# Kernel optimization log

Measured on AMD Instinct MI355X. Metric: run time of the kernel, lower is better.

The kernel has to match this reference:

```python
import jax, jax.numpy as jnp
import numpy as np
import math

T, N, D, H = 1024, 8, 1024, 16
HD = D // H  # head_dim = 64


def setup_inputs() -> dict:
    key = jax.random.key(0)
    k1, k2, k3, k4 = jax.random.split(key, 4)
    scale = 1.0 / math.sqrt(D)  # roughly xavier-scale params
    return {
        "x": jax.random.normal(k1, (T, N, D), dtype=jnp.float32),
        "q_weight": jax.random.normal(k2, (D, H, HD), dtype=jnp.float32) * scale,
        "v_weight": jax.random.normal(k3, (D, H, HD), dtype=jnp.float32) * scale,
        "out_w": jax.random.normal(k4, (D, D), dtype=jnp.float32) * scale,
        "out_b": jnp.zeros((D,), dtype=jnp.float32),
    }


def reference(x, q_weight, v_weight, out_w, out_b):
    inv_sqrt_hd = 1.0 / math.sqrt(HD)
    # q = k : (T, N, H, HD)
    q = jnp.einsum('tbm,mhd->tbhd', x, q_weight)
    q_sq = jnp.einsum('tbhd,tbhd->tbh', q, q)  # squared norms
    # squared L2 distance logits: (T, S, N, H)
    squared_dist = q_sq[:, None] + q_sq[None, :] - 2.0 * jnp.einsum('tbhd,sbhd->tsbh', q, q)
    attn_logits = -squared_dist * inv_sqrt_hd
    attn_weights = jax.nn.softmax(attn_logits, axis=1)  # softmax over source dim S
    # A = W_q W_q^T per head: (H, D, D)
    A = jnp.einsum('mhd,nhd->hmn', q_weight, q_weight) * inv_sqrt_hd
    XA = jnp.einsum('tbm,hmn->tbhn', x, A)           # (T, N, H, D)
    PXA = jnp.einsum('tsbh,sbhm->tbhm', attn_weights, XA)  # (T, N, H, D)
    PXAV = jnp.einsum('tbhm,mhd->tbhd', PXA, v_weight).reshape(T, N, D)
    return PXAV @ out_w.T + out_b
```

## Files before the change

### kernel.cpp

```cpp
#include <hip/hip_runtime.h>
#include <hip/hip_bf16.h>

#define T_ 1024
#define N_ 8
#define D_ 1024
#define H_ 16
#define HD_ 64

typedef __attribute__((ext_vector_type(8))) short bf16x8;
typedef __attribute__((ext_vector_type(4))) float f32x4;
typedef __attribute__((ext_vector_type(16))) float f32x16;
typedef __attribute__((ext_vector_type(4))) int i32x4;
typedef __attribute__((ext_vector_type(2))) int i32x2;
typedef unsigned short u16;
typedef unsigned int u32;

__device__ __forceinline__ float bf2f(u16 u){
  union { float f; unsigned int i; } v; v.i = ((unsigned int)u) << 16; return v.f;
}
__device__ __forceinline__ u16 f2bf(float f){
  union { float f; unsigned int i; } v; v.f = f;
  unsigned int r = v.i + 0x7FFFu + ((v.i >> 16) & 1u);
  return (u16)(r >> 16);
}
__device__ __forceinline__ u16 f2bf_fast(float f){
  __hip_bfloat16 h = __float2bfloat16(f);
  return *reinterpret_cast<u16*>(&h);
}
__device__ __forceinline__ float exp2_raw(float x){
  float r;
  asm("v_exp_f32 %0, %1" : "=v"(r) : "v"(x));
  return r;
}
__device__ __forceinline__ void gl_lds16(const u16* g, u16* l){
  __builtin_amdgcn_global_load_lds(
      (const __attribute__((address_space(1))) unsigned int*)g,
      (__attribute__((address_space(3))) unsigned int*)(unsigned int)(unsigned long long)l,
      16, 0, 0);
}

__global__ __launch_bounds__(256) void k_wqt(const float* __restrict__ Wq, u16* __restrict__ Wqt){
  __shared__ float tld[64][65];
  int m0 = blockIdx.x * 64, n0 = blockIdx.y * 64;
  int col = threadIdx.x & 63, rq = threadIdx.x >> 6;
  #pragma unroll
  for (int p = 0; p < 16; ++p){
    int row = rq * 16 + p;
    tld[row][col] = Wq[(size_t)(m0 + row) * D_ + n0 + col];
  }
  __syncthreads();
  #pragma unroll
  for (int p = 0; p < 16; ++p){
    int row = rq * 16 + p;
    Wqt[(size_t)(n0 + row) * D_ + m0 + col] = f2bf(tld[col][row]);
  }
}

__global__ __launch_bounds__(256) void k_bmatp(const float* __restrict__ qw, const float* __restrict__ vw,
                                               float* __restrict__ Bp){
  int h = (int)blockIdx.x >> 3, sp = (int)blockIdx.x & 7;
  int tid = threadIdx.x, lane = tid & 63, w = tid >> 6;
  int g = lane >> 4, c = lane & 15;
  __shared__ u16 Qt[64 * 72];
  __shared__ u16 Vt[64 * 72];
  f32x4 zero = {0.f, 0.f, 0.f, 0.f};
  f32x4 acc[4];
  #pragma unroll
  for (int eb = 0; eb < 4; ++eb) acc[eb] = zero;
  int m = tid >> 2, cg = tid & 3;
  for (int mt = sp * 128; mt < sp * 128 + 128; mt += 64){
    __syncthreads();
    #pragma unroll
    for (int q = 0; q < 4; ++q){
      int e0 = cg * 16 + q * 4;
      f32x4 vq = *(const f32x4*)(qw + (size_t)(mt + m) * D_ + h * 64 + e0);
      f32x4 vv = *(const f32x4*)(vw + (size_t)(mt + m) * D_ + h * 64 + e0);
      #pragma unroll
      for (int j = 0; j < 4; ++j){
        Qt[(e0 + j) * 72 + m] = f2bf_fast(vq[j]);
        Vt[(e0 + j) * 72 + m] = f2bf_fast(vv[j]);
      }
    }
    __syncthreads();
    #pragma unroll
    for (int kk = 0; kk < 2; ++kk){
      bf16x8 av = *(const bf16x8*)&Vt[(w * 16 + c) * 72 + kk * 32 + g * 8];
      #pragma unroll
      for (int eb = 0; eb < 4; ++eb){
        bf16x8 bq = *(const bf16x8*)&Qt[(eb * 16 + c) * 72 + kk * 32 + g * 8];
        acc[eb] = __builtin_amdgcn_mfma_f32_16x16x32_bf16(av, bq, acc[eb], 0, 0, 0);
      }
    }
  }
  #pragma unroll
  for (int eb = 0; eb < 4; ++eb)
    #pragma unroll
    for (int r = 0; r < 4; ++r){
      int d = w * 16 + g * 4 + r, e = eb * 16 + c;
      Bp[(((size_t)sp * 16 + h) * 64 + d) * 64 + e] = acc[eb][r];
    }
}

__global__ __launch_bounds__(256) void k_bred(const float* __restrict__ Bp, u16* __restrict__ Bt){
  int i = blockIdx.x * 256 + threadIdx.x;
  float s = 0.f;
  #pragma unroll
  for (int j = 0; j < 8; ++j) s += Bp[(size_t)j * 65536 + i];
  Bt[i] = f2bf(s * 0.125f);
}

__device__ __forceinline__ int swz(int row, int colbyte){
  return row * 64 + (((colbyte) ^ ((row & 7) << 4)) >> 1);
}

template<int A_F32, int B_F32, int EPI>
__global__ __launch_bounds__(256) void k_gemm(const void* __restrict__ A_, const void* __restrict__ B_,
                                              void* __restrict__ Cv, const float* __restrict__ bias,
                                              int M, int N, int K){
  int nbn = N >> 7;
  int ii = (int)blockIdx.x;
  int sw = (ii & 7) * 64 + (ii >> 3);
  int bm = sw / nbn, bn = sw % nbn;
  int tid = threadIdx.x, lane = tid & 63, wid = tid >> 6;
  int wr = wid >> 1, wc = wid & 1, g = lane >> 4, c = lane & 15;
  __shared__ u16 As[2][128 * 64];
  __shared__ u16 Bs[2][128 * 64];
  int srow[4], scol[4], sdst[4];
  #pragma unroll
  for (int p = 0; p < 4; ++p){
    int slot = (wid * 4 + p) * 64 + lane;
    int row = slot >> 3, c8 = slot & 7;
    srow[p] = row;
    scol[p] = (c8 ^ (row & 7)) * 8;
    sdst[p] = slot * 8;
  }
  int rrow[4], rc8[4];
  #pragma unroll
  for (int p = 0; p < 4; ++p){
    int ci = tid + p * 256;
    rrow[p] = ci >> 3; rc8[p] = ci & 7;
  }
  f32x4 zero = {0.f, 0.f, 0.f, 0.f};
  f32x4 acc[4][4];
  #pragma unroll
  for (int m = 0; m < 4; ++m)
    #pragma unroll
    for (int n = 0; n < 4; ++n) acc[m][n] = zero;
  f32x4 rA[4][2], rB[4][2];
  const u16* Ab = (const u16*)A_;
  const u16* Bb = (const u16*)B_;
  const float* Af = (const float*)A_;
  const float* Bf = (const float*)B_;
  if (!A_F32){
    #pragma unroll
    for (int p = 0; p < 4; ++p)
      gl_lds16(Ab + (size_t)(bm * 128 + srow[p]) * K + scol[p], &As[0][sdst[p]]);
  }
  if (!B_F32){
    #pragma unroll
    for (int p = 0; p < 4; ++p)
      gl_lds16(Bb + (size_t)(bn * 128 + srow[p]) * K + scol[p], &Bs[0][sdst[p]]);
  }
  if (A_F32){
    #pragma unroll
    for (int p = 0; p < 4; ++p){
      const float* src = Af + (size_t)(bm * 128 + rrow[p]) * K + rc8[p] * 8;
      rA[p][0] = *(const f32x4*)src;
      rA[p][1] = *(const f32x4*)(src + 4);
    }
    #pragma unroll
    for (int p = 0; p < 4; ++p){
      union { u16 u[8]; i32x4 v; } pk;
      #pragma unroll
      for (int j = 0; j < 4; ++j){ pk.u[j] = f2bf_fast(rA[p][0][j]); pk.u[4 + j] = f2bf_fast(rA[p][1][j]); }
      *(i32x4*)&As[0][swz(rrow[p], rc8[p] * 16)] = pk.v;
    }
  }
  if (B_F32){
    #pragma unroll
    for (int p = 0; p < 4; ++p){
      const float* src = Bf + (size_t)(bn * 128 + rrow[p]) * K + rc8[p] * 8;
      rB[p][0] = *(const f32x4*)src;
      rB[p][1] = *(const f32x4*)(src + 4);
    }
    #pragma unroll
    for (int p = 0; p < 4; ++p){
      union { u16 u[8]; i32x4 v; } pk;
      #pragma unroll
      for (int j = 0; j < 4; ++j){ pk.u[j] = f2bf_fast(rB[p][0][j]); pk.u[4 + j] = f2bf_fast(rB[p][1][j]); }
      *(i32x4*)&Bs[0][swz(rrow[p], rc8[p] * 16)] = pk.v;
    }
  }
  int NT = K >> 6;
  int cur = 0;
  for (int st = 0; st < NT; ++st){
    __syncthreads();
    int kt1 = (st + 1) * 64;
    int nb = cur ^ 1;
    if (st + 1 < NT){
      if (!A_F32){
        #pragma unroll
        for (int p = 0; p < 4; ++p)
          gl_lds16(Ab + (size_t)(bm * 128 + srow[p]) * K + kt1 + scol[p], &As[nb][sdst[p]]);
      }
      if (!B_F32){
        #pragma unroll
        for (int p = 0; p < 4; ++p)
          gl_lds16(Bb + (size_t)(bn * 128 + srow[p]) * K + kt1 + scol[p], &Bs[nb][sdst[p]]);
      }
      if (A_F32){
        #pragma unroll
        for (int p = 0; p < 4; ++p){
          const float* src = Af + (size_t)(bm * 128 + rrow[p]) * K + kt1 + rc8[p] * 8;
          rA[p][0] = *(const f32x4*)src;
          rA[p][1] = *(const f32x4*)(src + 4);
        }
      }
      if (B_F32){
        #pragma unroll
        for (int p = 0; p < 4; ++p){
          const float* src = Bf + (size_t)(bn * 128 + rrow[p]) * K + kt1 + rc8[p] * 8;
          rB[p][0] = *(const f32x4*)src;
          rB[p][1] = *(const f32x4*)(src + 4);
        }
      }
    }
    #pragma unroll
    for (int kk = 0; kk < 2; ++kk){
      bf16x8 af[4], bfr[4];
      #pragma unroll
      for (int m = 0; m < 4; ++m){
        int row = wr * 64 + m * 16 + c;
        af[m] = *(const bf16x8*)&As[cur][swz(row, kk * 64 + g * 16)];
      }
      #pragma unroll
      for (int n = 0; n < 4; ++n){
        int row = wc * 64 + n * 16 + c;
        bfr[n] = *(const bf16x8*)&Bs[cur][swz(row, kk * 64 + g * 16)];
      }
      #pragma unroll
      for (int m = 0; m < 4; ++m)
        #pragma unroll
        for (int n = 0; n < 4; ++n)
          acc[m][n] = __builtin_amdgcn_mfma_f32_16x16x32_bf16(af[m], bfr[n], acc[m][n], 0, 0, 0);
    }
    if (st + 1 < NT){
      if (A_F32){
        #pragma unroll
        for (int p = 0; p < 4; ++p){
          union { u16 u[8]; i32x4 v; } pk;
          #pragma unroll
          for (int j = 0; j < 4; ++j){ pk.u[j] = f2bf_fast(rA[p][0][j]); pk.u[4 + j] = f2bf_fast(rA[p][1][j]); }
          *(i32x4*)&As[nb][swz(rrow[p], rc8[p] * 16)] = pk.v;
        }
      }
      if (B_F32){
        #pragma unroll
        for (int p = 0; p < 4; ++p){
          union { u16 u[8]; i32x4 v; } pk;
          #pragma unroll
          for (int j = 0; j < 4; ++j){ pk.u[j] = f2bf_fast(rB[p][0][j]); pk.u[4 + j] = f2bf_fast(rB[p][1][j]); }
          *(i32x4*)&Bs[nb][swz(rrow[p], rc8[p] * 16)] = pk.v;
        }
      }
    }
    cur ^= 1;
  }
  #pragma unroll
  for (int m = 0; m < 4; ++m)
    #pragma unroll
    for (int n = 0; n < 4; ++n)
      #pragma unroll
      for (int r = 0; r < 4; ++r){
        int row = bm * 128 + wr * 64 + m * 16 + g * 4 + r;
        int col = bn * 128 + wc * 64 + n * 16 + c;
        float v = acc[m][n][r];
        if (EPI == 0){
          int t = row >> 3, b = row & 7, hh = col >> 6, dd = col & 63;
          ((u16*)Cv)[(((size_t)(b * H_ + hh)) * T_ + t) * HD_ + dd] = f2bf(v);
        } else {
          ((float*)Cv)[(size_t)row * N + col] = v + bias[col];
        }
      }
}

__global__ __launch_bounds__(256) void k_u(const u16* __restrict__ qb, const u16* __restrict__ Bt,
                                           u16* __restrict__ ubt, float* __restrict__ qsq){
  int blk = (int)blockIdx.x;
  int bh = blk >> 2;
  int w = threadIdx.x >> 6;
  int tt = (blk & 3) * 4 + w;
  int h = bh & 15, t0 = tt * 64;
  int lane = threadIdx.x & 63, g = lane >> 4, c = lane & 15;
  const float QS_SCALE = 0.125f * 1.44269504088896340736f;
  bf16x8 af[4][2], bq[4][2];
  #pragma unroll
  for (int mf = 0; mf < 4; ++mf)
    #pragma unroll
    for (int kk = 0; kk < 2; ++kk)
      af[mf][kk] = *(const bf16x8*)(Bt + ((size_t)(h * 64 + mf * 16 + c)) * 64 + kk * 32 + g * 8);
  #pragma unroll
  for (int nf = 0; nf < 4; ++nf)
    #pragma unroll
    for (int kk = 0; kk < 2; ++kk)
      bq[nf][kk] = *(const bf16x8*)(qb + ((size_t)(bh * 1024 + t0 + nf * 16 + c)) * 64 + kk * 32 + g * 8);
  #pragma unroll
  for (int nf = 0; nf < 4; ++nf){
    float ss = 0.f;
    #pragma unroll
    for (int kk = 0; kk < 2; ++kk)
      #pragma unroll
      for (int j = 0; j < 8; ++j){ float f = bf2f((u16)bq[nf][kk][j]); ss = fmaf(f, f, ss); }
    ss += __shfl_xor(ss, 16);
    ss += __shfl_xor(ss, 32);
    if (lane < 16) qsq[(size_t)bh * 1024 + t0 + nf * 16 + lane] = ss * QS_SCALE;
  }
  f32x4 zero = {0.f, 0.f, 0.f, 0.f};
  f32x4 acc[4][4];
  #pragma unroll
  for (int mf = 0; mf < 4; ++mf)
    #pragma unroll
    for (int nf = 0; nf < 4; ++nf) acc[mf][nf] = zero;
  #pragma unroll
  for (int kk = 0; kk < 2; ++kk)
    #pragma unroll
    for (int mf = 0; mf < 4; ++mf)
      #pragma unroll
      for (int nf = 0; nf < 4; ++nf)
        acc[mf][nf] = __builtin_amdgcn_mfma_f32_16x16x32_bf16(af[mf][kk], bq[nf][kk], acc[mf][nf], 0, 0, 0);
  #pragma unroll
  for (int mf = 0; mf < 4; ++mf)
    #pragma unroll
    for (int nf = 0; nf < 4; ++nf)
      #pragma unroll
      for (int r = 0; r < 4; ++r)
        ubt[((size_t)(bh * 64 + mf * 16 + g * 4 + r)) * 1024 + t0 + nf * 16 + c] = f2bf(acc[mf][nf][r]);
}

__global__ __launch_bounds__(256, 4) void k_attn(const u16* __restrict__ qb, const u16* __restrict__ ubt,
                                                 const float* __restrict__ qsq, u16* __restrict__ obm){
  int i = (int)blockIdx.x;
  int bh = ((i & 7) << 4) + (i >> 6);
  int tt = (i >> 3) & 7;
  int b = bh >> 4, h = bh & 15;
  int tid = threadIdx.x, w = tid >> 6, lane = tid & 63;
  int lo = lane & 31, hi = lane >> 5;
  __shared__ u16 Kl[2][64 * 64];
  __shared__ u16 Ul[2][64 * 64];
  __shared__ float Qs[1024];
  const float C1 = 0.25f * 1.44269504088896340736f;
  int t0 = tt * 128 + w * 32;
  const u16* qbh = qb + (size_t)bh * 65536;
  const u16* ubh = ubt + (size_t)bh * 65536;
  const float* qsb = qsq + (size_t)bh * 1024;
  *(f32x4*)&Qs[tid * 4] = *(const f32x4*)(qsb + tid * 4);
  bf16x8 qB[4];
  #pragma unroll
  for (int kd = 0; kd < 4; ++kd)
    qB[kd] = *(const bf16x8*)(qbh + (t0 + lo) * 64 + kd * 16 + hi * 8);
  f32x16 o0 = {0,0,0,0,0,0,0,0,0,0,0,0,0,0,0,0};
  f32x16 o1 = {0,0,0,0,0,0,0,0,0,0,0,0,0,0,0,0};
  const f32x16 zero16 = {0,0,0,0,0,0,0,0,0,0,0,0,0,0,0,0};
  float l_c = 0.f;
  int slot0 = (w * 2 + 0) * 64 + lane, slot1 = (w * 2 + 1) * 64 + lane;
  int r0 = slot0 >> 3, sc0 = ((slot0 & 7) ^ (r0 & 7)) * 8;
  int r1 = slot1 >> 3, sc1 = ((slot1 & 7) ^ (r1 & 7)) * 8;
  int d0 = (w * 2 + 0) * 512, d1 = (w * 2 + 1) * 512;
  gl_lds16(qbh + r0 * 64 + sc0, &Kl[0][d0]);
  gl_lds16(qbh + r1 * 64 + sc1, &Kl[0][d1]);
  gl_lds16(ubh + (size_t)r0 * 1024 + sc0, &Ul[0][d0]);
  gl_lds16(ubh + (size_t)r1 * 1024 + sc1, &Ul[0][d1]);
  int cur = 0;
  for (int st = 0; st < 16; ++st){
    int s0 = st * 64;
    __syncthreads();
    if (st < 15){
      int s1 = s0 + 64;
      int nb = cur ^ 1;
      gl_lds16(qbh + (s1 + r0) * 64 + sc0, &Kl[nb][d0]);
      gl_lds16(qbh + (s1 + r1) * 64 + sc1, &Kl[nb][d1]);
      gl_lds16(ubh + (size_t)r0 * 1024 + s1 + sc0, &Ul[nb][d0]);
      gl_lds16(ubh + (size_t)r1 * 1024 + s1 + sc1, &Ul[nb][d1]);
    }
    const u16* Kc = &Kl[cur][0];
    const u16* Uc = &Ul[cur][0];
    #pragma unroll
    for (int ts = 0; ts < 2; ++ts){
      f32x16 sf = zero16;
      __builtin_amdgcn_s_setprio(1);
      #pragma unroll
      for (int kd = 0; kd < 4; ++kd){
        bf16x8 kA = *(const bf16x8*)&Kc[swz(ts * 32 + lo, kd * 32 + hi * 16)];
        sf = __builtin_amdgcn_mfma_f32_32x32x16_bf16(kA, qB[kd], sf, 0, 0, 0);
      }
      __builtin_amdgcn_s_setprio(0);
      f32x4 qs_[4];
      #pragma unroll
      for (int q = 0; q < 4; ++q)
        qs_[q] = *(const f32x4*)&Qs[s0 + ts * 32 + q * 8 + hi * 4];
      float p[16];
      #pragma unroll
      for (int r = 0; r < 16; ++r)
        p[r] = exp2_raw(fmaf(sf[r], C1, -qs_[r >> 2][r & 3]));
      float sA = ((p[0] + p[1]) + (p[2] + p[3])) + ((p[4] + p[5]) + (p[6] + p[7]));
      float sB = ((p[8] + p[9]) + (p[10] + p[11])) + ((p[12] + p[13]) + (p[14] + p[15]));
      l_c += sA + sB;
      u32 W[8];
      #pragma unroll
      for (int q = 0; q < 8; ++q)
        W[q] = ((u32)f2bf_fast(p[2 * q + 1]) << 16) | (u32)f2bf_fast(p[2 * q]);
      #pragma unroll
      for (int ml = 0; ml < 2; ++ml){
        int m_g = ts * 2 + ml;
        int base = ml * 4;
        i32x2 sw0 = __builtin_amdgcn_permlane32_swap((int)W[base + 0], (int)W[base + 2], false, false);
        i32x2 sw1 = __builtin_amdgcn_permlane32_swap((int)W[base + 1], (int)W[base + 3], false, false);
        union { u32 wd[4]; bf16x8 v; } pa;
        pa.wd[0] = (u32)sw0[0]; pa.wd[1] = (u32)sw1[0]; pa.wd[2] = (u32)sw0[1]; pa.wd[3] = (u32)sw1[1];
        bf16x8 u0 = *(const bf16x8*)&Uc[swz(lo, m_g * 32 + hi * 16)];
        bf16x8 u1 = *(const bf16x8*)&Uc[swz(32 + lo, m_g * 32 + hi * 16)];
        __builtin_amdgcn_s_setprio(1);
        o0 = __builtin_amdgcn_mfma_f32_32x32x16_bf16(pa.v, u0, o0, 0, 0, 0);
        o1 = __builtin_amdgcn_mfma_f32_32x32x16_bf16(pa.v, u1, o1, 0, 0, 0);
        __builtin_amdgcn_s_setprio(0);
      }
    }
    cur ^= 1;
  }
  l_c += __shfl_xor(l_c, 32);
  float inv = 1.0f / l_c;
  #pragma unroll
  for (int r = 0; r < 16; ++r){
    int tr = (r & 3) + 8 * (r >> 2) + 4 * hi;
    float invr = __shfl(inv, tr);
    size_t rowb = ((size_t)((t0 + tr) * 8 + b)) * 1024 + h * 64;
    obm[rowb + lo] = f2bf(o0[r] * invr);
    obm[rowb + 32 + lo] = f2bf(o1[r] * invr);
  }
}

extern "C" void kernel_launch(void* const* d_in, const int* in_sizes, int n_in,
                              void* d_out, int out_size, void* d_ws, size_t ws_size,
                              hipStream_t stream) {
  const float* x   = (const float*)d_in[0];
  const float* qw  = (const float*)d_in[1];
  const float* vw  = (const float*)d_in[2];
  const float* ow  = (const float*)d_in[3];
  const float* ob_bias = (const float*)d_in[4];
  float* out = (float*)d_out;

  float* Bp = (float*)d_out;
  u16* qb  = (u16*)d_out;
  u16* ubt = (u16*)((char*)d_out + (size_t)16 * 1024 * 1024);

  char* ws = (char*)d_ws;
  size_t off = 0;
  auto alloc = [&](size_t bytes) -> void* {
    void* p = ws + off;
    off += (bytes + 255) & ~(size_t)255;
    return p;
  };
  u16*   wqt = (u16*)  alloc((size_t)1024 * 1024 * 2);
  u16*   obm = (u16*)  alloc((size_t)8192 * 1024 * 2);
  float* qsq = (float*)alloc((size_t)128 * 1024 * 4);
  u16*   Bt  = (u16*)  alloc((size_t)16 * 64 * 64 * 2);

  k_bmatp<<<128, 256, 0, stream>>>(qw, vw, Bp);
  k_bred<<<256, 256, 0, stream>>>(Bp, Bt);
  k_wqt<<<dim3(16, 16), 256, 0, stream>>>(qw, wqt);
  k_gemm<1, 0, 0><<<512, 256, 0, stream>>>(x, wqt, qb, nullptr, 8192, 1024, 1024);
  k_u<<<512, 256, 0, stream>>>(qb, Bt, ubt, qsq);
  k_attn<<<1024, 256, 0, stream>>>(qb, ubt, qsq, obm);
  k_gemm<0, 1, 1><<<512, 256, 0, stream>>>(obm, ow, out, ob_bias, 8192, 1024, 1024);
}
```

Before: 127.8 us.

## Merge weight-prep kernels and double attention block size to share K/U tiles

Combines the B-matrix partial product kernel and the Wq transpose kernel into a single launch, selecting the branch by block index, which removes one kernel launch. The attention kernel moves to 512-thread blocks covering 256 query rows, so each block's K/U tile loads into LDS serve twice as many query rows and each thread issues half as many async loads. The cost is fewer blocks (512), a lower occupancy bound, and a larger LDS footprint in the merged prep kernel.

```diff
diff --git a/kernel.cpp b/kernel.cpp
--- a/kernel.cpp
+++ b/kernel.cpp
@@ -8,6 +8,7 @@
 #define HD_ 64
 
 typedef __attribute__((ext_vector_type(8))) short bf16x8;
+typedef __attribute__((ext_vector_type(2))) float f32x2;
 typedef __attribute__((ext_vector_type(4))) float f32x4;
 typedef __attribute__((ext_vector_type(16))) float f32x16;
 typedef __attribute__((ext_vector_type(4))) int i32x4;
@@ -39,66 +40,70 @@
       16, 0, 0);
 }
 
-__global__ __launch_bounds__(256) void k_wqt(const float* __restrict__ Wq, u16* __restrict__ Wqt){
-  __shared__ float tld[64][65];
-  int m0 = blockIdx.x * 64, n0 = blockIdx.y * 64;
-  int col = threadIdx.x & 63, rq = threadIdx.x >> 6;
-  #pragma unroll
-  for (int p = 0; p < 16; ++p){
-    int row = rq * 16 + p;
-    tld[row][col] = Wq[(size_t)(m0 + row) * D_ + n0 + col];
-  }
-  __syncthreads();
-  #pragma unroll
-  for (int p = 0; p < 16; ++p){
-    int row = rq * 16 + p;
-    Wqt[(size_t)(n0 + row) * D_ + m0 + col] = f2bf(tld[col][row]);
-  }
-}
-
-__global__ __launch_bounds__(256) void k_bmatp(const float* __restrict__ qw, const float* __restrict__ vw,
-                                               float* __restrict__ Bp){
-  int h = (int)blockIdx.x >> 3, sp = (int)blockIdx.x & 7;
-  int tid = threadIdx.x, lane = tid & 63, w = tid >> 6;
-  int g = lane >> 4, c = lane & 15;
+__global__ __launch_bounds__(256) void k_pre(const float* __restrict__ qw, const float* __restrict__ vw,
+                                             float* __restrict__ Bp, const float* __restrict__ Wq,
+                                             u16* __restrict__ Wqt){
   __shared__ u16 Qt[64 * 72];
   __shared__ u16 Vt[64 * 72];
-  f32x4 zero = {0.f, 0.f, 0.f, 0.f};
-  f32x4 acc[4];
-  #pragma unroll
-  for (int eb = 0; eb < 4; ++eb) acc[eb] = zero;
-  int m = tid >> 2, cg = tid & 3;
-  for (int mt = sp * 128; mt < sp * 128 + 128; mt += 64){
+  __shared__ float tld[64][65];
+  int blk = (int)blockIdx.x;
+  int tid = threadIdx.x;
+  if (blk < 128){
+    int h = blk >> 3, sp = blk & 7;
+    int lane = tid & 63, w = tid >> 6;
+    int g = lane >> 4, c = lane & 15;
+    f32x4 zero = {0.f, 0.f, 0.f, 0.f};
+    f32x4 acc[4];
+    #pragma unroll
+    for (int eb = 0; eb < 4; ++eb) acc[eb] = zero;
+    int m = tid >> 2, cg = tid & 3;
+    for (int mt = sp * 128; mt < sp * 128 + 128; mt += 64){
+      __syncthreads();
+      #pragma unroll
+      for (int q = 0; q < 4; ++q){
+        int e0 = cg * 16 + q * 4;
+        f32x4 vq = *(const f32x4*)(qw + (size_t)(mt + m) * D_ + h * 64 + e0);
+        f32x4 vv = *(const f32x4*)(vw + (size_t)(mt + m) * D_ + h * 64 + e0);
+        #pragma unroll
+        for (int j = 0; j < 4; ++j){
+          Qt[(e0 + j) * 72 + m] = f2bf_fast(vq[j]);
+          Vt[(e0 + j) * 72 + m] = f2bf_fast(vv[j]);
+        }
+      }
+      __syncthreads();
+      #pragma unroll
+      for (int kk = 0; kk < 2; ++kk){
+        bf16x8 av = *(const bf16x8*)&Vt[(w * 16 + c) * 72 + kk * 32 + g * 8];
+        #pragma unroll
+        for (int eb = 0; eb < 4; ++eb){
+          bf16x8 bq = *(const bf16x8*)&Qt[(eb * 16 + c) * 72 + kk * 32 + g * 8];
+          acc[eb] = __builtin_amdgcn_mfma_f32_16x16x32_bf16(av, bq, acc[eb], 0, 0, 0);
+        }
+      }
+    }
+    #pragma unroll
+    for (int eb = 0; eb < 4; ++eb)
+      #pragma unroll
+      for (int r = 0; r < 4; ++r){
+        int d = w * 16 + g * 4 + r, e = eb * 16 + c;
+        Bp[(((size_t)sp * 16 + h) * 64 + d) * 64 + e] = acc[eb][r];
+      }
+  } else {
+    int b2 = blk - 128;
+    int m0 = (b2 & 15) * 64, n0 = (b2 >> 4) * 64;
+    int col = tid & 63, rq = tid >> 6;
+    #pragma unroll
+    for (int p = 0; p < 16; ++p){
+      int row = rq * 16 + p;
+      tld[row][col] = Wq[(size_t)(m0 + row) * D_ + n0 + col];
+    }
     __syncthreads();
     #pragma unroll
-    for (int q = 0; q < 4; ++q){
-      int e0 = cg * 16 + q * 4;
-      f32x4 vq = *(const f32x4*)(qw + (size_t)(mt + m) * D_ + h * 64 + e0);
-      f32x4 vv = *(const f32x4*)(vw + (size_t)(mt + m) * D_ + h * 64 + e0);
-      #pragma unroll
-      for (int j = 0; j < 4; ++j){
-        Qt[(e0 + j) * 72 + m] = f2bf_fast(vq[j]);
-        Vt[(e0 + j) * 72 + m] = f2bf_fast(vv[j]);
-      }
-    }
-    __syncthreads();
-    #pragma unroll
-    for (int kk = 0; kk < 2; ++kk){
-      bf16x8 av = *(const bf16x8*)&Vt[(w * 16 + c) * 72 + kk * 32 + g * 8];
-      #pragma unroll
-      for (int eb = 0; eb < 4; ++eb){
-        bf16x8 bq = *(const bf16x8*)&Qt[(eb * 16 + c) * 72 + kk * 32 + g * 8];
-        acc[eb] = __builtin_amdgcn_mfma_f32_16x16x32_bf16(av, bq, acc[eb], 0, 0, 0);
-      }
-    }
-  }
-  #pragma unroll
-  for (int eb = 0; eb < 4; ++eb)
-    #pragma unroll
-    for (int r = 0; r < 4; ++r){
-      int d = w * 16 + g * 4 + r, e = eb * 16 + c;
-      Bp[(((size_t)sp * 16 + h) * 64 + d) * 64 + e] = acc[eb][r];
-    }
+    for (int p = 0; p < 16; ++p){
+      int row = rq * 16 + p;
+      Wqt[(size_t)(n0 + row) * D_ + m0 + col] = f2bf(tld[col][row]);
+    }
+  }
 }
 
 __global__ __launch_bounds__(256) void k_bred(const float* __restrict__ Bp, u16* __restrict__ Bt){
@@ -337,11 +342,11 @@
         ubt[((size_t)(bh * 64 + mf * 16 + g * 4 + r)) * 1024 + t0 + nf * 16 + c] = f2bf(acc[mf][nf][r]);
 }
 
-__global__ __launch_bounds__(256, 4) void k_attn(const u16* __restrict__ qb, const u16* __restrict__ ubt,
+__global__ __launch_bounds__(512, 2) void k_attn(const u16* __restrict__ qb, const u16* __restrict__ ubt,
                                                  const float* __restrict__ qsq, u16* __restrict__ obm){
   int i = (int)blockIdx.x;
-  int bh = ((i & 7) << 4) + (i >> 6);
-  int tt = (i >> 3) & 7;
+  int bh = ((i & 7) << 4) + (i >> 5);
+  int tt = (i >> 3) & 3;
   int b = bh >> 4, h = bh & 15;
   int tid = threadIdx.x, w = tid >> 6, lane = tid & 63;
   int lo = lane & 31, hi = lane >> 5;
@@ -349,11 +354,11 @@
   __shared__ u16 Ul[2][64 * 64];
   __shared__ float Qs[1024];
   const float C1 = 0.25f * 1.44269504088896340736f;
-  int t0 = tt * 128 + w * 32;
+  int t0 = tt * 256 + w * 32;
   const u16* qbh = qb + (size_t)bh * 65536;
   const u16* ubh = ubt + (size_t)bh * 65536;
   const float* qsb = qsq + (size_t)bh * 1024;
-  *(f32x4*)&Qs[tid * 4] = *(const f32x4*)(qsb + tid * 4);
+  *(f32x2*)&Qs[tid * 2] = *(const f32x2*)(qsb + tid * 2);
   bf16x8 qB[4];
   #pragma unroll
   for (int kd = 0; kd < 4; ++kd)
@@ -362,14 +367,10 @@
   f32x16 o1 = {0,0,0,0,0,0,0,0,0,0,0,0,0,0,0,0};
   const f32x16 zero16 = {0,0,0,0,0,0,0,0,0,0,0,0,0,0,0,0};
   float l_c = 0.f;
-  int slot0 = (w * 2 + 0) * 64 + lane, slot1 = (w * 2 + 1) * 64 + lane;
-  int r0 = slot0 >> 3, sc0 = ((slot0 & 7) ^ (r0 & 7)) * 8;
-  int r1 = slot1 >> 3, sc1 = ((slot1 & 7) ^ (r1 & 7)) * 8;
-  int d0 = (w * 2 + 0) * 512, d1 = (w * 2 + 1) * 512;
+  int r0 = tid >> 3, sc0 = ((tid & 7) ^ (r0 & 7)) * 8;
+  int d0 = w * 512;
   gl_lds16(qbh + r0 * 64 + sc0, &Kl[0][d0]);
-  gl_lds16(qbh + r1 * 64 + sc1, &Kl[0][d1]);
   gl_lds16(ubh + (size_t)r0 * 1024 + sc0, &Ul[0][d0]);
-  gl_lds16(ubh + (size_t)r1 * 1024 + sc1, &Ul[0][d1]);
   int cur = 0;
   for (int st = 0; st < 16; ++st){
     int s0 = st * 64;
@@ -378,9 +379,7 @@
       int s1 = s0 + 64;
       int nb = cur ^ 1;
       gl_lds16(qbh + (s1 + r0) * 64 + sc0, &Kl[nb][d0]);
-      gl_lds16(qbh + (s1 + r1) * 64 + sc1, &Kl[nb][d1]);
       gl_lds16(ubh + (size_t)r0 * 1024 + s1 + sc0, &Ul[nb][d0]);
-      gl_lds16(ubh + (size_t)r1 * 1024 + s1 + sc1, &Ul[nb][d1]);
     }
     const u16* Kc = &Kl[cur][0];
     const u16* Uc = &Ul[cur][0];
@@ -465,11 +464,10 @@
   float* qsq = (float*)alloc((size_t)128 * 1024 * 4);
   u16*   Bt  = (u16*)  alloc((size_t)16 * 64 * 64 * 2);
 
-  k_bmatp<<<128, 256, 0, stream>>>(qw, vw, Bp);
+  k_pre<<<384, 256, 0, stream>>>(qw, vw, Bp, qw, wqt);
   k_bred<<<256, 256, 0, stream>>>(Bp, Bt);
-  k_wqt<<<dim3(16, 16), 256, 0, stream>>>(qw, wqt);
   k_gemm<1, 0, 0><<<512, 256, 0, stream>>>(x, wqt, qb, nullptr, 8192, 1024, 1024);
   k_u<<<512, 256, 0, stream>>>(qb, Bt, ubt, qsq);
-  k_attn<<<1024, 256, 0, stream>>>(qb, ubt, qsq, obm);
+  k_attn<<<512, 512, 0, stream>>>(qb, ubt, qsq, obm);
   k_gemm<0, 1, 1><<<512, 256, 0, stream>>>(obm, ow, out, ob_bias, 8192, 1024, 1024);
 }
```

After: 121.8 us. 4.7% less time.
